# Kernel tuning notes

Hardware: AMD Instinct MI355X
Metric: run time of the kernel (lower is better)

## Reference

```python
import jax, jax.numpy as jnp
import numpy as np

EPS = 1e-7  # utils.add_dummy(eps=True) dummy value


def setup_inputs() -> dict:
    key = jax.random.key(0)
    ks = jax.random.split(key, 8)
    n_mentions, emb = 8192, 1024
    batch, n_ants, pw_emb = 1024, 50, 64
    pair_emb = 3 * emb + pw_emb  # 3136
    hidden = 1024
    return {
        "all_mentions": jax.random.normal(ks[0], (n_mentions, emb), jnp.float32),
        "mentions_batch": jax.random.normal(ks[1], (batch, emb), jnp.float32),
        "pw_batch": jax.random.normal(ks[2], (batch, n_ants, pw_emb), jnp.float32),
        "top_rough_scores_batch": jax.random.normal(ks[3], (batch, n_ants), jnp.float32),
        "W1": jax.random.normal(ks[4], (pair_emb, hidden), jnp.float32) * 0.02,
        "b1": jnp.zeros((hidden,), jnp.float32),
        "W_out": jax.random.normal(ks[5], (hidden, 1), jnp.float32) * 0.02,
        "b_out": jnp.zeros((1,), jnp.float32),
        "top_indices_batch": jax.random.randint(ks[6], (batch, n_ants), 0, n_mentions, jnp.int64),
    }


def reference(all_mentions, mentions_batch, pw_batch, top_rough_scores_batch,
              W1, b1, W_out, b_out, top_indices_batch):
    # gather antecedent embeddings: [batch, n_ants, emb]
    b_mentions = all_mentions[top_indices_batch]
    a_mentions = jnp.broadcast_to(mentions_batch[:, None, :], b_mentions.shape)
    # pair matrix: [batch, n_ants, 3*emb + pw_emb]
    pair = jnp.concatenate([a_mentions, b_mentions, a_mentions * b_mentions, pw_batch], axis=2)
    # FFNN: Linear -> LeakyReLU (dropout is identity in eval) -> Linear(->1)
    h = jax.nn.leaky_relu(jnp.einsum("bnf,fh->bnh", pair, W1) + b1, negative_slope=0.01)
    ffnn = (jnp.einsum("bnh,ho->bno", h, W_out) + b_out)[..., 0]  # [batch, n_ants]
    scores = top_rough_scores_batch + ffnn
    dummy = jnp.full((scores.shape[0], 1), EPS, scores.dtype)
    return jnp.concatenate([dummy, scores], axis=1)  # [batch, n_ants + 1]
```

## Files before the change

### kernel.cpp

```cpp
#include <hip/hip_runtime.h>
#include <cstdint>


typedef short short8 __attribute__((ext_vector_type(8)));
typedef float f32x4 __attribute__((ext_vector_type(4)));

#define BT_STRIDE 100352
#define MT_STRIDE 32768
#define PT_STRIDE 34816

static __device__ __forceinline__ unsigned short f2bf(float x) {
  union { float f; unsigned u; } v; v.f = x;
  unsigned r = v.u + 0x7fffu + ((v.u >> 16) & 1u);
  return (unsigned short)(r >> 16);
}
static __device__ __forceinline__ float bf2f(unsigned short u) {
  union { unsigned u; float f; } v; v.u = ((unsigned)u) << 16;
  return v.f;
}
static __device__ __forceinline__ float rbf(float x) {
  return bf2f(f2bf(x));
}

__global__ void k_pack(const float* __restrict__ W1, const float* __restrict__ am,
                       const float* __restrict__ allm,
                       unsigned short* __restrict__ BtAll,
                       unsigned short* __restrict__ Mt) {
  int bid = blockIdx.x;
  if (bid < 784) {
    __shared__ float t[64][65];
    int k0 = (bid % 49) * 64, n0 = (bid / 49) * 64;
    int c = threadIdx.x & 63, r4 = threadIdx.x >> 6;
#pragma unroll
    for (int rr = 0; rr < 16; ++rr) {
      int r = rr * 4 + r4;
      t[r][c] = W1[(size_t)(k0 + r) * 1024 + n0 + c];
    }
    __syncthreads();
#pragma unroll
    for (int qq = 0; qq < 2; ++qq) {
      int q = threadIdx.x * 2 + qq;
      int cc = q >> 3, rg = q & 7;
      short8 v;
#pragma unroll
      for (int e = 0; e < 8; ++e) v[e] = (short)f2bf(t[rg * 8 + e][cc]);
      int ct = (n0 + cc) >> 4;
      int kc = (k0 >> 5) + (rg >> 2);
      int ln = (cc & 15) + ((rg & 3) << 4);
      *(short8*)((char*)BtAll + (size_t)ct * BT_STRIDE + kc * 1024 + ln * 16) = v;
    }
  } else {
    int rt = bid - 784, t = threadIdx.x;
    const float* S = (rt < 512) ? (allm + (size_t)rt * 16 * 1024)
                                : (am + (size_t)(rt - 512) * 16 * 1024);
    int pf = t & 15, oct = (t >> 4) & 3, kcl = t >> 6;
    const float* row = S + (size_t)pf * 1024;
    char* dst = (char*)Mt + (size_t)rt * MT_STRIDE + (t & 63) * 16;
#pragma unroll
    for (int pass = 0; pass < 8; ++pass) {
      int kc = pass * 4 + kcl;
      int k = kc * 32 + oct * 8;
      float4 v0 = *(const float4*)(row + k);
      float4 v1 = *(const float4*)(row + k + 4);
      short8 o;
      o[0] = (short)f2bf(v0.x); o[1] = (short)f2bf(v0.y);
      o[2] = (short)f2bf(v0.z); o[3] = (short)f2bf(v0.w);
      o[4] = (short)f2bf(v1.x); o[5] = (short)f2bf(v1.y);
      o[6] = (short)f2bf(v1.z); o[7] = (short)f2bf(v1.w);
      *(short8*)(dst + kc * 1024) = o;
    }
  }
}

__global__ void k_cvt(const float* __restrict__ s, unsigned short* __restrict__ d, int n4) {
  int i = blockIdx.x * 256 + threadIdx.x;
  if (i < n4) {
    float4 v = ((const float4*)s)[i];
    ushort4 o; o.x = f2bf(v.x); o.y = f2bf(v.y); o.z = f2bf(v.z); o.w = f2bf(v.w);
    ((ushort4*)d)[i] = o;
  }
}

__global__ void k_pairs(const float* __restrict__ am,
                        const unsigned short* __restrict__ Aball,
                        const float* __restrict__ pw, const int* __restrict__ idx,
                        unsigned short* __restrict__ Pt) {
  __shared__ int g16[16];
  int rt = blockIdx.x, t = threadIdx.x;
  if (t < 16) g16[t] = idx[rt * 16 + t];
  __syncthreads();
  int pf = t & 15, oct = (t >> 4) & 3, kcl = t >> 6;
  int p = rt * 16 + pf;
  const float* arow = am + (size_t)(p / 50) * 1024;
  const unsigned short* brow = Aball + (size_t)g16[pf] * 1024;
  char* dst = (char*)Pt + (size_t)rt * PT_STRIDE + (t & 63) * 16;
#pragma unroll
  for (int pass = 0; pass < 8; ++pass) {
    int kc = pass * 4 + kcl;
    int k = kc * 32 + oct * 8;
    float4 a0 = *(const float4*)(arow + k);
    float4 a1 = *(const float4*)(arow + k + 4);
    short8 b8 = *(const short8*)(brow + k);
    short8 o;
    o[0] = (short)f2bf(rbf(a0.x) * bf2f((unsigned short)b8[0]));
    o[1] = (short)f2bf(rbf(a0.y) * bf2f((unsigned short)b8[1]));
    o[2] = (short)f2bf(rbf(a0.z) * bf2f((unsigned short)b8[2]));
    o[3] = (short)f2bf(rbf(a0.w) * bf2f((unsigned short)b8[3]));
    o[4] = (short)f2bf(rbf(a1.x) * bf2f((unsigned short)b8[4]));
    o[5] = (short)f2bf(rbf(a1.y) * bf2f((unsigned short)b8[5]));
    o[6] = (short)f2bf(rbf(a1.z) * bf2f((unsigned short)b8[6]));
    o[7] = (short)f2bf(rbf(a1.w) * bf2f((unsigned short)b8[7]));
    *(short8*)(dst + kc * 1024) = o;
  }
  if (t < 128) {
    int kc = 32 + (t >> 6);
    int kpw = (t >> 6) * 32 + oct * 8;
    const float* prow = pw + (size_t)p * 64;
    float4 v0 = *(const float4*)(prow + kpw);
    float4 v1 = *(const float4*)(prow + kpw + 4);
    short8 o;
    o[0] = (short)f2bf(v0.x); o[1] = (short)f2bf(v0.y);
    o[2] = (short)f2bf(v0.z); o[3] = (short)f2bf(v0.w);
    o[4] = (short)f2bf(v1.x); o[5] = (short)f2bf(v1.y);
    o[6] = (short)f2bf(v1.z); o[7] = (short)f2bf(v1.w);
    *(short8*)(dst + kc * 1024) = o;
  }
}

template <int MODE>
__global__ __launch_bounds__(256, 2) void k_gt(
    const unsigned short* __restrict__ At, const unsigned short* __restrict__ BtAll,
    float* __restrict__ C, float* __restrict__ partial,
    const float* __restrict__ Hab, const float* __restrict__ b1,
    const float* __restrict__ Wout, const int* __restrict__ idx) {
  constexpr int NKC = MODE ? 34 : 32;
  constexpr int A_STRIDE = MODE ? PT_STRIDE : MT_STRIDE;
  int tid = threadIdx.x, lane = tid & 63, wave = tid >> 6;
  int llo = lane & 15, lhi = lane >> 4;
  int id = blockIdx.x;
  int x, y;
  if (MODE == 1) {
    int r = id >> 3;
    x = (id & 7) * 100 + (r >> 1);
    y = r & 1;
  } else {
    x = id >> 1;
    y = id & 1;
  }
  int kcoff = MODE ? 64 : ((x < 128) ? 32 : 0);
  int row0 = x * 64;
  int n0w = y * 512 + wave * 128;
  const char* pa = (const char*)At + (size_t)(row0 >> 4) * A_STRIDE + lane * 16;
  const char* pb = (const char*)BtAll + (size_t)(n0w >> 4) * BT_STRIDE +
                   (size_t)kcoff * 1024 + lane * 16;

  f32x4 acc[4][8] = {};
  short8 aA[4], bA[8], aB[4], bB[8];
#pragma unroll
  for (int m = 0; m < 4; ++m) aA[m] = *(const short8*)(pa + (size_t)m * A_STRIDE);
#pragma unroll
  for (int n = 0; n < 8; ++n) bA[n] = *(const short8*)(pb + (size_t)n * BT_STRIDE);
  for (int kt = 0; kt < NKC; kt += 2) {
#pragma unroll
    for (int m = 0; m < 4; ++m)
      aB[m] = *(const short8*)(pa + (size_t)m * A_STRIDE + (kt + 1) * 1024);
#pragma unroll
    for (int n = 0; n < 8; ++n)
      bB[n] = *(const short8*)(pb + (size_t)n * BT_STRIDE + (kt + 1) * 1024);
#pragma unroll
    for (int m = 0; m < 4; ++m)
#pragma unroll
      for (int n = 0; n < 8; ++n)
        acc[m][n] = __builtin_amdgcn_mfma_f32_16x16x32_bf16(aA[m], bA[n], acc[m][n], 0, 0, 0);
    if (kt + 2 < NKC) {
#pragma unroll
      for (int m = 0; m < 4; ++m)
        aA[m] = *(const short8*)(pa + (size_t)m * A_STRIDE + (kt + 2) * 1024);
#pragma unroll
      for (int n = 0; n < 8; ++n)
        bA[n] = *(const short8*)(pb + (size_t)n * BT_STRIDE + (kt + 2) * 1024);
    }
#pragma unroll
    for (int m = 0; m < 4; ++m)
#pragma unroll
      for (int n = 0; n < 8; ++n)
        acc[m][n] = __builtin_amdgcn_mfma_f32_16x16x32_bf16(aB[m], bB[n], acc[m][n], 0, 0, 0);
  }

  if (MODE == 0) {
#pragma unroll
    for (int m = 0; m < 4; ++m)
#pragma unroll
      for (int i = 0; i < 4; ++i) {
        int row = row0 + m * 16 + lhi * 4 + i;
#pragma unroll
        for (int n = 0; n < 8; ++n)
          C[(size_t)row * 1024 + n0w + n * 16 + llo] = acc[m][n][i];
      }
  } else {
    float b1v[8], wov[8];
    int coln[8];
#pragma unroll
    for (int n = 0; n < 8; ++n) {
      coln[n] = n0w + n * 16 + llo;
      b1v[n] = b1[coln[n]];
      wov[n] = Wout[coln[n]];
    }
    int chunk = n0w >> 6;
#pragma unroll
    for (int m = 0; m < 4; ++m)
#pragma unroll
      for (int i = 0; i < 4; ++i) {
        int p = row0 + m * 16 + lhi * 4 + i;
        int bb = p / 50;
        int gg = idx[p];
        const float* Har = Hab + (size_t)(8192 + bb) * 1024;
        const float* Hbr = Hab + (size_t)gg * 1024;
        float s0 = 0.f, s1 = 0.f;
#pragma unroll
        for (int n = 0; n < 4; ++n) {
          float h = acc[m][n][i] + Har[coln[n]] + Hbr[coln[n]] + b1v[n];
          h = h > 0.f ? h : 0.01f * h;
          s0 += h * wov[n];
        }
#pragma unroll
        for (int n = 4; n < 8; ++n) {
          float h = acc[m][n][i] + Har[coln[n]] + Hbr[coln[n]] + b1v[n];
          h = h > 0.f ? h : 0.01f * h;
          s1 += h * wov[n];
        }
        s0 += __shfl_xor(s0, 1, 64);
        s0 += __shfl_xor(s0, 2, 64);
        s0 += __shfl_xor(s0, 4, 64);
        s0 += __shfl_xor(s0, 8, 64);
        s1 += __shfl_xor(s1, 1, 64);
        s1 += __shfl_xor(s1, 2, 64);
        s1 += __shfl_xor(s1, 4, 64);
        s1 += __shfl_xor(s1, 8, 64);
        if (llo == 0) {
          partial[(size_t)p * 16 + chunk + 0] = s0;
          partial[(size_t)p * 16 + chunk + 1] = s1;
        }
      }
  }
}

__global__ void k_final(const float* __restrict__ partial, const float* __restrict__ rough,
                        const float* __restrict__ bout, float* __restrict__ out) {
  int t = blockIdx.x * 256 + threadIdx.x;
  if (t < 51200) {
    float s = rough[t] + bout[0];
    const float* pp = partial + (size_t)t * 16;
#pragma unroll
    for (int c = 0; c < 16; ++c) s += pp[c];
    out[(size_t)(t / 50) * 51 + 1 + (t % 50)] = s;
  }
  if (t < 1024) out[(size_t)t * 51] = 1e-7f;
}

extern "C" void kernel_launch(void* const* d_in, const int* in_sizes, int n_in,
                              void* d_out, int out_size, void* d_ws, size_t ws_size,
                              hipStream_t stream) {
  (void)in_sizes; (void)n_in; (void)out_size;
  const float* allm  = (const float*)d_in[0];
  const float* am    = (const float*)d_in[1];
  const float* pw    = (const float*)d_in[2];
  const float* rough = (const float*)d_in[3];
  const float* W1    = (const float*)d_in[4];
  const float* b1    = (const float*)d_in[5];
  const float* Wout  = (const float*)d_in[6];
  const float* bout  = (const float*)d_in[7];
  const int*   idx   = (const int*)d_in[8];
  float* out = (float*)d_out;

  char* w = (char*)d_ws;
  unsigned short* BtAll = (unsigned short*)w; w += (size_t)64 * BT_STRIDE;
  unsigned short* Mt    = (unsigned short*)w; w += (size_t)576 * MT_STRIDE;
  unsigned short* Aball = (unsigned short*)w; w += (size_t)8192 * 1024 * 2;
  unsigned short* Pt    = (unsigned short*)w; w += (size_t)3200 * PT_STRIDE;
  float* Hab            = (float*)w;          w += (size_t)9216 * 1024 * 4;
  float* part           = (float*)w;          w += (size_t)51200 * 16 * 4;
  size_t need = (size_t)(w - (char*)d_ws);
  if (ws_size < need) return;

  k_pack<<<dim3(1360), 256, 0, stream>>>(W1, am, allm, BtAll, Mt);
  k_cvt<<<dim3(8192), 256, 0, stream>>>(allm, Aball, 8192 * 1024 / 4);
  k_pairs<<<dim3(3200), 256, 0, stream>>>(am, Aball, pw, idx, Pt);
  k_gt<0><<<dim3(288), 256, 0, stream>>>(Mt, BtAll, Hab, nullptr,
                                         nullptr, nullptr, nullptr, nullptr);
  k_gt<1><<<dim3(1600), 256, 0, stream>>>(Pt, BtAll, nullptr, part,
                                          Hab, b1, Wout, idx);
  k_final<<<dim3(200), 256, 0, stream>>>(part, rough, bout, out);
}
```

Baseline: 247.9 us.

## Merge independent prep kernels and overlap Hab GEMM with pair building

Folds the bf16 conversion of all_mentions into the packing kernel as extra blocks, and combines the Hab GEMM (gt0) with pair-matrix construction in one launch, since the two have no dependency on each other. This cuts launches from six to four and lets the small 288-block GEMM run alongside the memory-bound pair-building blocks instead of serially. The merged kernel carries the GEMM's launch bounds and register footprint, which may lower occupancy for the pairs blocks.

Result: faster. 227.4 us (-8.3%).

```diff
diff --git a/kernel.cpp b/kernel.cpp
--- a/kernel.cpp
+++ b/kernel.cpp
@@ -22,10 +22,10 @@
   return bf2f(f2bf(x));
 }
 
-__global__ void k_pack(const float* __restrict__ W1, const float* __restrict__ am,
-                       const float* __restrict__ allm,
-                       unsigned short* __restrict__ BtAll,
-                       unsigned short* __restrict__ Mt) {
+__global__ __launch_bounds__(256) void k_prep(
+    const float* __restrict__ W1, const float* __restrict__ am,
+    const float* __restrict__ allm, unsigned short* __restrict__ BtAll,
+    unsigned short* __restrict__ Mt, unsigned short* __restrict__ Aball) {
   int bid = blockIdx.x;
   if (bid < 784) {
     __shared__ float t[64][65];
@@ -49,7 +49,7 @@
       int ln = (cc & 15) + ((rg & 3) << 4);
       *(short8*)((char*)BtAll + (size_t)ct * BT_STRIDE + kc * 1024 + ln * 16) = v;
     }
-  } else {
+  } else if (bid < 1360) {
     int rt = bid - 784, t = threadIdx.x;
     const float* S = (rt < 512) ? (allm + (size_t)rt * 16 * 1024)
                                 : (am + (size_t)(rt - 512) * 16 * 1024);
@@ -69,24 +69,77 @@
       o[6] = (short)f2bf(v1.z); o[7] = (short)f2bf(v1.w);
       *(short8*)(dst + kc * 1024) = o;
     }
-  }
-}
-
-__global__ void k_cvt(const float* __restrict__ s, unsigned short* __restrict__ d, int n4) {
-  int i = blockIdx.x * 256 + threadIdx.x;
-  if (i < n4) {
-    float4 v = ((const float4*)s)[i];
-    ushort4 o; o.x = f2bf(v.x); o.y = f2bf(v.y); o.z = f2bf(v.z); o.w = f2bf(v.w);
-    ((ushort4*)d)[i] = o;
-  }
-}
-
-__global__ void k_pairs(const float* __restrict__ am,
-                        const unsigned short* __restrict__ Aball,
-                        const float* __restrict__ pw, const int* __restrict__ idx,
-                        unsigned short* __restrict__ Pt) {
+  } else {
+    int i = (bid - 1360) * 256 + threadIdx.x;
+    if (i < 8192 * 1024 / 4) {
+      float4 v = ((const float4*)allm)[i];
+      ushort4 o; o.x = f2bf(v.x); o.y = f2bf(v.y); o.z = f2bf(v.z); o.w = f2bf(v.w);
+      ((ushort4*)Aball)[i] = o;
+    }
+  }
+}
+
+static __device__ __forceinline__ void gt0_body(
+    int id, const unsigned short* __restrict__ Mt,
+    const unsigned short* __restrict__ BtAll, float* __restrict__ Hab) {
+  int tid = threadIdx.x, lane = tid & 63, wave = tid >> 6;
+  int llo = lane & 15, lhi = lane >> 4;
+  int x = id >> 1, y = id & 1;
+  int kcoff = (x < 128) ? 32 : 0;
+  int row0 = x * 64;
+  int n0w = y * 512 + wave * 128;
+  const char* pa = (const char*)Mt + (size_t)(row0 >> 4) * MT_STRIDE + lane * 16;
+  const char* pb = (const char*)BtAll + (size_t)(n0w >> 4) * BT_STRIDE +
+                   (size_t)kcoff * 1024 + lane * 16;
+  f32x4 acc[4][8] = {};
+  short8 aA[4], bA[8], aB[4], bB[8];
+#pragma unroll
+  for (int m = 0; m < 4; ++m) aA[m] = *(const short8*)(pa + (size_t)m * MT_STRIDE);
+#pragma unroll
+  for (int n = 0; n < 8; ++n) bA[n] = *(const short8*)(pb + (size_t)n * BT_STRIDE);
+  for (int kt = 0; kt < 32; kt += 2) {
+#pragma unroll
+    for (int m = 0; m < 4; ++m)
+      aB[m] = *(const short8*)(pa + (size_t)m * MT_STRIDE + (kt + 1) * 1024);
+#pragma unroll
+    for (int n = 0; n < 8; ++n)
+      bB[n] = *(const short8*)(pb + (size_t)n * BT_STRIDE + (kt + 1) * 1024);
+#pragma unroll
+    for (int m = 0; m < 4; ++m)
+#pragma unroll
+      for (int n = 0; n < 8; ++n)
+        acc[m][n] = __builtin_amdgcn_mfma_f32_16x16x32_bf16(aA[m], bA[n], acc[m][n], 0, 0, 0);
+    if (kt + 2 < 32) {
+#pragma unroll
+      for (int m = 0; m < 4; ++m)
+        aA[m] = *(const short8*)(pa + (size_t)m * MT_STRIDE + (kt + 2) * 1024);
+#pragma unroll
+      for (int n = 0; n < 8; ++n)
+        bA[n] = *(const short8*)(pb + (size_t)n * BT_STRIDE + (kt + 2) * 1024);
+    }
+#pragma unroll
+    for (int m = 0; m < 4; ++m)
+#pragma unroll
+      for (int n = 0; n < 8; ++n)
+        acc[m][n] = __builtin_amdgcn_mfma_f32_16x16x32_bf16(aB[m], bB[n], acc[m][n], 0, 0, 0);
+  }
+#pragma unroll
+  for (int m = 0; m < 4; ++m)
+#pragma unroll
+    for (int i = 0; i < 4; ++i) {
+      int row = row0 + m * 16 + lhi * 4 + i;
+#pragma unroll
+      for (int n = 0; n < 8; ++n)
+        Hab[(size_t)row * 1024 + n0w + n * 16 + llo] = acc[m][n][i];
+    }
+}
+
+static __device__ __forceinline__ void pairs_body(
+    int rt, const float* __restrict__ am, const unsigned short* __restrict__ Aball,
+    const float* __restrict__ pw, const int* __restrict__ idx,
+    unsigned short* __restrict__ Pt) {
   __shared__ int g16[16];
-  int rt = blockIdx.x, t = threadIdx.x;
+  int t = threadIdx.x;
   if (t < 16) g16[t] = idx[rt * 16 + t];
   __syncthreads();
   int pf = t & 15, oct = (t >> 4) & 3, kcl = t >> 6;
@@ -127,43 +180,42 @@
   }
 }
 
-template <int MODE>
-__global__ __launch_bounds__(256, 2) void k_gt(
-    const unsigned short* __restrict__ At, const unsigned short* __restrict__ BtAll,
-    float* __restrict__ C, float* __restrict__ partial,
-    const float* __restrict__ Hab, const float* __restrict__ b1,
-    const float* __restrict__ Wout, const int* __restrict__ idx) {
-  constexpr int NKC = MODE ? 34 : 32;
-  constexpr int A_STRIDE = MODE ? PT_STRIDE : MT_STRIDE;
+__global__ __launch_bounds__(256, 2) void k_mid(
+    const unsigned short* __restrict__ Mt, const unsigned short* __restrict__ BtAll,
+    float* __restrict__ Hab, const float* __restrict__ am,
+    const unsigned short* __restrict__ Aball, const float* __restrict__ pw,
+    const int* __restrict__ idx, unsigned short* __restrict__ Pt) {
+  if (blockIdx.x < 288) gt0_body(blockIdx.x, Mt, BtAll, Hab);
+  else pairs_body(blockIdx.x - 288, am, Aball, pw, idx, Pt);
+}
+
+__global__ __launch_bounds__(256, 2) void k_main(
+    const unsigned short* __restrict__ Pt, const unsigned short* __restrict__ BtAll,
+    float* __restrict__ partial, const float* __restrict__ Hab,
+    const float* __restrict__ b1, const float* __restrict__ Wout,
+    const int* __restrict__ idx) {
   int tid = threadIdx.x, lane = tid & 63, wave = tid >> 6;
   int llo = lane & 15, lhi = lane >> 4;
   int id = blockIdx.x;
-  int x, y;
-  if (MODE == 1) {
-    int r = id >> 3;
-    x = (id & 7) * 100 + (r >> 1);
-    y = r & 1;
-  } else {
-    x = id >> 1;
-    y = id & 1;
-  }
-  int kcoff = MODE ? 64 : ((x < 128) ? 32 : 0);
+  int r = id >> 3;
+  int x = (id & 7) * 100 + (r >> 1);
+  int y = r & 1;
   int row0 = x * 64;
   int n0w = y * 512 + wave * 128;
-  const char* pa = (const char*)At + (size_t)(row0 >> 4) * A_STRIDE + lane * 16;
+  const char* pa = (const char*)Pt + (size_t)(row0 >> 4) * PT_STRIDE + lane * 16;
   const char* pb = (const char*)BtAll + (size_t)(n0w >> 4) * BT_STRIDE +
-                   (size_t)kcoff * 1024 + lane * 16;
+                   (size_t)64 * 1024 + lane * 16;
 
   f32x4 acc[4][8] = {};
   short8 aA[4], bA[8], aB[4], bB[8];
 #pragma unroll
-  for (int m = 0; m < 4; ++m) aA[m] = *(const short8*)(pa + (size_t)m * A_STRIDE);
+  for (int m = 0; m < 4; ++m) aA[m] = *(const short8*)(pa + (size_t)m * PT_STRIDE);
 #pragma unroll
   for (int n = 0; n < 8; ++n) bA[n] = *(const short8*)(pb + (size_t)n * BT_STRIDE);
-  for (int kt = 0; kt < NKC; kt += 2) {
-#pragma unroll
-    for (int m = 0; m < 4; ++m)
-      aB[m] = *(const short8*)(pa + (size_t)m * A_STRIDE + (kt + 1) * 1024);
+  for (int kt = 0; kt < 34; kt += 2) {
+#pragma unroll
+    for (int m = 0; m < 4; ++m)
+      aB[m] = *(const short8*)(pa + (size_t)m * PT_STRIDE + (kt + 1) * 1024);
 #pragma unroll
     for (int n = 0; n < 8; ++n)
       bB[n] = *(const short8*)(pb + (size_t)n * BT_STRIDE + (kt + 1) * 1024);
@@ -172,10 +224,10 @@
 #pragma unroll
       for (int n = 0; n < 8; ++n)
         acc[m][n] = __builtin_amdgcn_mfma_f32_16x16x32_bf16(aA[m], bA[n], acc[m][n], 0, 0, 0);
-    if (kt + 2 < NKC) {
+    if (kt + 2 < 34) {
 #pragma unroll
       for (int m = 0; m < 4; ++m)
-        aA[m] = *(const short8*)(pa + (size_t)m * A_STRIDE + (kt + 2) * 1024);
+        aA[m] = *(const short8*)(pa + (size_t)m * PT_STRIDE + (kt + 2) * 1024);
 #pragma unroll
       for (int n = 0; n < 8; ++n)
         bA[n] = *(const short8*)(pb + (size_t)n * BT_STRIDE + (kt + 2) * 1024);
@@ -187,62 +239,50 @@
         acc[m][n] = __builtin_amdgcn_mfma_f32_16x16x32_bf16(aB[m], bB[n], acc[m][n], 0, 0, 0);
   }
 
-  if (MODE == 0) {
-#pragma unroll
-    for (int m = 0; m < 4; ++m)
-#pragma unroll
-      for (int i = 0; i < 4; ++i) {
-        int row = row0 + m * 16 + lhi * 4 + i;
-#pragma unroll
-        for (int n = 0; n < 8; ++n)
-          C[(size_t)row * 1024 + n0w + n * 16 + llo] = acc[m][n][i];
+  float b1v[8], wov[8];
+  int coln[8];
+#pragma unroll
+  for (int n = 0; n < 8; ++n) {
+    coln[n] = n0w + n * 16 + llo;
+    b1v[n] = b1[coln[n]];
+    wov[n] = Wout[coln[n]];
+  }
+  int chunk = n0w >> 6;
+#pragma unroll
+  for (int m = 0; m < 4; ++m)
+#pragma unroll
+    for (int i = 0; i < 4; ++i) {
+      int p = row0 + m * 16 + lhi * 4 + i;
+      int bb = p / 50;
+      int gg = idx[p];
+      const float* Har = Hab + (size_t)(8192 + bb) * 1024;
+      const float* Hbr = Hab + (size_t)gg * 1024;
+      float s0 = 0.f, s1 = 0.f;
+#pragma unroll
+      for (int n = 0; n < 4; ++n) {
+        float h = acc[m][n][i] + Har[coln[n]] + Hbr[coln[n]] + b1v[n];
+        h = h > 0.f ? h : 0.01f * h;
+        s0 += h * wov[n];
       }
-  } else {
-    float b1v[8], wov[8];
-    int coln[8];
-#pragma unroll
-    for (int n = 0; n < 8; ++n) {
-      coln[n] = n0w + n * 16 + llo;
-      b1v[n] = b1[coln[n]];
-      wov[n] = Wout[coln[n]];
-    }
-    int chunk = n0w >> 6;
-#pragma unroll
-    for (int m = 0; m < 4; ++m)
-#pragma unroll
-      for (int i = 0; i < 4; ++i) {
-        int p = row0 + m * 16 + lhi * 4 + i;
-        int bb = p / 50;
-        int gg = idx[p];
-        const float* Har = Hab + (size_t)(8192 + bb) * 1024;
-        const float* Hbr = Hab + (size_t)gg * 1024;
-        float s0 = 0.f, s1 = 0.f;
-#pragma unroll
-        for (int n = 0; n < 4; ++n) {
-          float h = acc[m][n][i] + Har[coln[n]] + Hbr[coln[n]] + b1v[n];
-          h = h > 0.f ? h : 0.01f * h;
-          s0 += h * wov[n];
-        }
-#pragma unroll
-        for (int n = 4; n < 8; ++n) {
-          float h = acc[m][n][i] + Har[coln[n]] + Hbr[coln[n]] + b1v[n];
-          h = h > 0.f ? h : 0.01f * h;
-          s1 += h * wov[n];
-        }
-        s0 += __shfl_xor(s0, 1, 64);
-        s0 += __shfl_xor(s0, 2, 64);
-        s0 += __shfl_xor(s0, 4, 64);
-        s0 += __shfl_xor(s0, 8, 64);
-        s1 += __shfl_xor(s1, 1, 64);
-        s1 += __shfl_xor(s1, 2, 64);
-        s1 += __shfl_xor(s1, 4, 64);
-        s1 += __shfl_xor(s1, 8, 64);
-        if (llo == 0) {
-          partial[(size_t)p * 16 + chunk + 0] = s0;
-          partial[(size_t)p * 16 + chunk + 1] = s1;
-        }
+#pragma unroll
+      for (int n = 4; n < 8; ++n) {
+        float h = acc[m][n][i] + Har[coln[n]] + Hbr[coln[n]] + b1v[n];
+        h = h > 0.f ? h : 0.01f * h;
+        s1 += h * wov[n];
       }
-  }
+      s0 += __shfl_xor(s0, 1, 64);
+      s0 += __shfl_xor(s0, 2, 64);
+      s0 += __shfl_xor(s0, 4, 64);
+      s0 += __shfl_xor(s0, 8, 64);
+      s1 += __shfl_xor(s1, 1, 64);
+      s1 += __shfl_xor(s1, 2, 64);
+      s1 += __shfl_xor(s1, 4, 64);
+      s1 += __shfl_xor(s1, 8, 64);
+      if (llo == 0) {
+        partial[(size_t)p * 16 + chunk + 0] = s0;
+        partial[(size_t)p * 16 + chunk + 1] = s1;
+      }
+    }
 }
 
 __global__ void k_final(const float* __restrict__ partial, const float* __restrict__ rough,
@@ -283,12 +323,8 @@
   size_t need = (size_t)(w - (char*)d_ws);
   if (ws_size < need) return;
 
-  k_pack<<<dim3(1360), 256, 0, stream>>>(W1, am, allm, BtAll, Mt);
-  k_cvt<<<dim3(8192), 256, 0, stream>>>(allm, Aball, 8192 * 1024 / 4);
-  k_pairs<<<dim3(3200), 256, 0, stream>>>(am, Aball, pw, idx, Pt);
-  k_gt<0><<<dim3(288), 256, 0, stream>>>(Mt, BtAll, Hab, nullptr,
-                                         nullptr, nullptr, nullptr, nullptr);
-  k_gt<1><<<dim3(1600), 256, 0, stream>>>(Pt, BtAll, nullptr, part,
-                                          Hab, b1, Wout, idx);
+  k_prep<<<dim3(9552), 256, 0, stream>>>(W1, am, allm, BtAll, Mt, Aball);
+  k_mid<<<dim3(3488), 256, 0, stream>>>(Mt, BtAll, Hab, am, Aball, pw, idx, Pt);
+  k_main<<<dim3(1600), 256, 0, stream>>>(Pt, BtAll, part, Hab, b1, Wout, idx);
   k_final<<<dim3(200), 256, 0, stream>>>(part, rough, bout, out);
 }
```
